# Kernel tuning notes

Measured on AMD Instinct MI355X. Metric: run time of the kernel, lower is better.

Reference implementation:

```python
import jax, jax.numpy as jnp
import numpy as np

RADIUS = 0.15
NSAMPLE = 128
NPOINT = 128
EPS = 1e-5  # BatchNorm eps (eval mode, running_mean=0, running_var=1)


def _bn(x, g, b):
    shape = (1, -1) + (1,) * (x.ndim - 2)
    return x * (g / jnp.sqrt(1.0 + EPS)).reshape(shape) + b.reshape(shape)


def _fps(x, npoint):
    # farthest point sampling; x: (Bk, N, 3) -> (Bk, npoint) int32
    Bn, N, _ = x.shape

    def step(carry, _):
        dist, far = carry
        c = jnp.take_along_axis(x, far[:, None, None], 1)  # (Bk,1,3)
        d = jnp.sum((x - c) ** 2, -1)
        dist = jnp.minimum(dist, d)
        return (dist, jnp.argmax(dist, -1).astype(jnp.int32)), far

    init = (jnp.full((Bn, N), 1e10, x.dtype), jnp.zeros((Bn,), jnp.int32))
    _, idxs = jax.lax.scan(step, init, None, length=npoint)
    return idxs.T  # (Bk, npoint)


def _sa_module(x, f, mlp):
    # PointnetSAModuleVotes: FPS -> ball query -> group (use_xyz, normalize_xyz)
    # -> shared MLP (conv2d 1x1 + BN + ReLU) -> max over nsample.
    Bk, M, _ = x.shape
    fps_idx = _fps(x, NPOINT)
    new_xyz = jnp.take_along_axis(x, fps_idx[..., None], 1)  # (Bk,np,3)
    d2 = jnp.sum((new_xyz[:, :, None, :] - x[:, None, :, :]) ** 2, -1)  # (Bk,np,M)
    cand = jnp.where(d2 < RADIUS ** 2, jnp.arange(M)[None, None, :], M)
    cand = jnp.sort(cand, -1)[..., :NSAMPLE]  # first nsample in-radius indices
    first = cand[..., :1]
    first = jnp.where(first == M, 0, first)
    idx = jnp.where(cand == M, first, cand)  # (Bk,np,ns), pad with first valid
    gx = jnp.take_along_axis(x, idx.reshape(Bk, -1)[..., None], 1).reshape(Bk, NPOINT, NSAMPLE, 3)
    gxn = (gx - new_xyz[:, :, None, :]) / RADIUS  # normalize_xyz=True
    gf = jnp.take_along_axis(f[:, :, None, :], idx[:, None, :, :], 3)  # (Bk,C,np,ns)
    h = jnp.concatenate([gxn.transpose(0, 3, 1, 2), gf], 1)  # (Bk, C+3, np, ns)
    for (w, b, g, be) in mlp:
        h = jax.nn.relu(_bn(jnp.einsum('oc,bcps->bops', w, h) + b[None, :, None, None], g, be))
    return new_xyz, h.max(-1)  # (Bk,np,3), (Bk,128,np)


def setup_inputs() -> dict:
    key = jax.random.key(0)
    ks = iter(jax.random.split(key, 40))
    B, M, K, C = 2, 1024, 19, 256
    inp = {}
    inp['xyz'] = jax.random.normal(next(ks), (B, M, K, 3), jnp.float32)
    inp['features'] = jax.random.normal(next(ks), (B, C, K, M), jnp.float32)

    def conv_p(prefix, cin, cout):
        inp[prefix + '_w'] = jax.random.normal(next(ks), (cout, cin), jnp.float32) * (1.0 / np.sqrt(cin))
        inp[prefix + '_b'] = jax.random.normal(next(ks), (cout,), jnp.float32) * 0.02
        inp[prefix + '_g'] = 1.0 + 0.1 * jax.random.normal(next(ks), (cout,), jnp.float32)
        inp[prefix + '_be'] = 0.02 * jax.random.normal(next(ks), (cout,), jnp.float32)

    conv_p('m1', C + 3, 128)  # use_xyz -> 259 in-channels
    conv_p('m2', 128, 128)
    conv_p('m3', 128, 128)
    conv_p('c1', 128, 128)
    conv_p('c2', 128, 128)
    inp['op_w'] = jax.random.normal(next(ks), (K, 5, 128), jnp.float32) * (1.0 / np.sqrt(128))
    inp['op_b'] = jax.random.normal(next(ks), (K, 5), jnp.float32) * 0.02
    return inp


def reference(xyz, features, m1_w, m1_b, m1_g, m1_be, m2_w, m2_b, m2_g, m2_be,
              m3_w, m3_b, m3_g, m3_be, c1_w, c1_b, c1_g, c1_be,
              c2_w, c2_b, c2_g, c2_be, op_w, op_b):
    B, M, K, _ = xyz.shape
    C = features.shape[1]
    # fold vote_factor k into the batch dim (all per-k SA/conv weights are shared)
    x = xyz.transpose(0, 2, 1, 3).reshape(B * K, M, 3)
    f = features.transpose(0, 2, 1, 3).reshape(B * K, C, M)
    mlp = [(m1_w, m1_b, m1_g, m1_be), (m2_w, m2_b, m2_g, m2_be), (m3_w, m3_b, m3_g, m3_be)]
    new_xyz, feat = _sa_module(x, f, mlp)
    net = jax.nn.relu(_bn(jnp.einsum('oc,bcp->bop', c1_w, feat) + c1_b[None, :, None], c1_g, c1_be))
    net = jax.nn.relu(_bn(jnp.einsum('oc,bcp->bop', c2_w, net) + c2_b[None, :, None], c2_g, c2_be))
    net = net.reshape(B, K, 128, NPOINT)
    # per-k output conv (conv_op ModuleList), 128 -> 2+3
    out = jnp.einsum('koc,bkcp->bkop', op_w, net) + op_b[None, :, :, None]
    net_t = out.transpose(0, 1, 3, 2)  # (B,K,np,5)
    agg_xyz = new_xyz.reshape(B, K, NPOINT, 3)
    center = agg_xyz + net_t[..., 2:5]  # decode_scores_
    scores = jnp.concatenate([net_t[..., :2], center], -1)  # obj(2) + center(3)
    return scores, agg_xyz, feat.reshape(B, K, 128, NPOINT)
```

## Files before the change

### kernel.cpp

```cpp
#include <hip/hip_runtime.h>
#include <math.h>

#define NBK   38

#define OFF_XC    0u
#define OFF_NXYZ  466944u
#define OFF_BIDX  525312u
#define OFF_W1F   3015680u
#define OFF_PREP  22938624u
#define OFF_WF    22955008u
#define OFF_CNT   23348224u

#define OUT_AGG   24320
#define OUT_FEAT  38912

typedef short bf16x8 __attribute__((ext_vector_type(8)));
typedef float f32x4  __attribute__((ext_vector_type(4)));
typedef int   v4i    __attribute__((ext_vector_type(4)));
typedef int   v2i    __attribute__((ext_vector_type(2)));

__device__ __forceinline__ float dist2f(float a0, float a1, float a2,
                                        float b0, float b1, float b2) {
#pragma clang fp contract(off)
  float d0 = a0 - b0;
  float d1 = a1 - b1;
  float d2 = a2 - b2;
  return d0 * d0 + d1 * d1 + d2 * d2;
}

__device__ __forceinline__ void split2rn(float v, unsigned& sh, unsigned& sm) {
  unsigned u = __float_as_uint(v);
  unsigned rh = (u + 0x7fffu + ((u >> 16) & 1u)) & 0xffff0000u;
  sh = rh >> 16;
  float r1 = v - __uint_as_float(rh);
  unsigned u1 = __float_as_uint(r1);
  unsigned rm = (u1 + 0x7fffu + ((u1 >> 16) & 1u)) & 0xffff0000u;
  sm = rm >> 16;
}

__global__ __launch_bounds__(1024, 4) void front_kernel(
    const float* __restrict__ xyz, const float* __restrict__ feats,
    const float* __restrict__ m1w, const float* __restrict__ m1b,
    const float* __restrict__ m1g, const float* __restrict__ m1be,
    const float* __restrict__ m2w, const float* __restrict__ m2b,
    const float* __restrict__ m2g, const float* __restrict__ m2be,
    const float* __restrict__ m3w, const float* __restrict__ m3b,
    const float* __restrict__ m3g, const float* __restrict__ m3be,
    const float* __restrict__ c1w, const float* __restrict__ c1b,
    const float* __restrict__ c1g, const float* __restrict__ c1be,
    const float* __restrict__ c2w, const float* __restrict__ c2b,
    const float* __restrict__ c2g, const float* __restrict__ c2be,
    float* __restrict__ xc, float* __restrict__ nxyz, float* __restrict__ agg,
    int* __restrict__ bidx, int* __restrict__ counts,
    float* __restrict__ W1f, short* __restrict__ Wf, float* __restrict__ prep)
{
  __shared__ __align__(16) char smem[32768];
  int bid = blockIdx.x, t = threadIdx.x;
  int wave = t >> 6, lane = t & 63;

  if (bid < NBK) {
    int bk = bid;
    int b = bk / 19, k = bk % 19;
    float* sx0 = (float*)smem;
    float* sx1 = sx0 + 1024;
    float* sx2 = sx1 + 1024;
    float* scen = sx2 + 1024;
    float* sd = scen + 384;
    int* si = (int*)(sd + 16);
    int* sfar = si + 16;

    const float* src = xyz + ((size_t)((b * 1024 + t) * 19 + k)) * 3;
    float x0 = src[0], x1 = src[1], x2 = src[2];
    sx0[t] = x0; sx1[t] = x1; sx2[t] = x2;
    xc[(bk * 3 + 0) * 1024 + t] = x0;
    xc[(bk * 3 + 1) * 1024 + t] = x1;
    xc[(bk * 3 + 2) * 1024 + t] = x2;
    if (t == 0) *sfar = 0;
    float dist = 1e10f;
    __syncthreads();

    for (int it = 0; it < 128; ++it) {
      int far = *sfar;
      float c0 = sx0[far], c1 = sx1[far], c2 = sx2[far];
      if (t < 3) scen[it * 3 + t] = (t == 0) ? c0 : ((t == 1) ? c1 : c2);
      float d = dist2f(x0, x1, x2, c0, c1, c2);
      dist = fminf(dist, d);
      float dmax = dist;
#pragma unroll
      for (int off = 1; off <= 32; off <<= 1)
        dmax = fmaxf(dmax, __shfl_xor(dmax, off));
      unsigned long long mk = __ballot(dist == dmax);
      if (lane == 0) {
        sd[wave] = dmax;
        si[wave] = (wave << 6) + __builtin_ctzll(mk);
      }
      __syncthreads();
      if (t < 16) {
        float dw = sd[t]; int iw = si[t];
        unsigned long long key =
            ((unsigned long long)__float_as_uint(dw) << 32) | (unsigned)(1023 - iw);
#pragma unroll
        for (int off = 8; off >= 1; off >>= 1) {
          unsigned hi = (unsigned)(key >> 32), lo = (unsigned)key;
          unsigned h2 = __shfl_xor(hi, off);
          unsigned l2 = __shfl_xor(lo, off);
          unsigned long long ok = ((unsigned long long)h2 << 32) | l2;
          if (ok > key) key = ok;
        }
        if (t == 0) *sfar = 1023 - (int)(key & 0xffffffffu);
      }
      __syncthreads();
    }

    if (t < 384) {
      float v = scen[t];
      nxyz[bk * 384 + t] = v;
      agg[bk * 384 + t]  = v;
    }

    for (int p = wave * 8; p < wave * 8 + 8; ++p) {
      float c0 = scen[p * 3 + 0], c1 = scen[p * 3 + 1], c2 = scen[p * 3 + 2];
      int* outp = bidx + ((size_t)(bk * 128 + p)) * 128;
      int count = 0, first = 0;
      bool got = false;
      for (int ch = 0; ch < 16 && count < 128; ++ch) {
        int m = (ch << 6) + lane;
        float d = dist2f(sx0[m], sx1[m], sx2[m], c0, c1, c2);
        bool flag = d < 0.0225f;
        unsigned long long mask = __ballot(flag);
        if (!got && mask) { first = (ch << 6) + __builtin_ctzll(mask); got = true; }
        int pos = count + (int)__popcll(mask & ((1ull << lane) - 1ull));
        if (flag && pos < 128) outp[pos] = m;
        count += (int)__popcll(mask);
      }
      for (int j = count + lane; j < 128; j += 64) outp[j] = first;
      if (lane == 0) counts[bk * 128 + p] = count > 128 ? 128 : count;
    }
    return;
  }

  if (bid < 342) {
    short* ffrag = (short*)smem;
    if (t >= 256) {
      for (int i = 0; i < 8; ++i) __syncthreads();
      return;
    }
    int blk = bid - NBK;
    int bk = blk >> 3, m0 = (blk & 7) << 7;
    int b = bk / 19, k = bk % 19;
    int quad = lane >> 4, nl = lane & 15;
    int mloc = t & 127, chalf = t >> 7;
    int st_w = mloc >> 4, sl_w = mloc & 15;
    const float* fbase = feats + ((size_t)(b * 4864 + k)) * 1024 + m0 + mloc;

    f32x4 acc[2][8];
#pragma unroll
    for (int oi = 0; oi < 2; ++oi)
#pragma unroll
      for (int st = 0; st < 8; ++st) acc[oi][st] = (f32x4){0.f, 0.f, 0.f, 0.f};

    for (int ch = 0; ch < 4; ++ch) {
      int cbase = ch * 64 + chalf * 32;
#pragma unroll
      for (int g = 0; g < 4; ++g) {
        float v[8];
#pragma unroll
        for (int j = 0; j < 8; ++j)
          v[j] = fbase[(size_t)(cbase + g * 8 + j) * 19456];
        unsigned sh[8], sm[8];
#pragma unroll
        for (int j = 0; j < 8; ++j) split2rn(v[j], sh[j], sm[j]);
        int base = chalf * 4096 + st_w * 512 + (g * 16 + sl_w) * 8;
        v4i ph = {(int)(sh[0] | (sh[1] << 16)), (int)(sh[2] | (sh[3] << 16)),
                  (int)(sh[4] | (sh[5] << 16)), (int)(sh[6] | (sh[7] << 16))};
        *(v4i*)&ffrag[base] = ph;
        v4i pm = {(int)(sm[0] | (sm[1] << 16)), (int)(sm[2] | (sm[3] << 16)),
                  (int)(sm[4] | (sm[5] << 16)), (int)(sm[6] | (sm[7] << 16))};
        *(v4i*)&ffrag[base + 8192] = pm;
      }
      __syncthreads();
#pragma unroll
      for (int kkl = 0; kkl < 2; ++kkl) {
        int kk = ch * 2 + kkl;
        bf16x8 a[2][2];
#pragma unroll
        for (int oi = 0; oi < 2; ++oi) {
          int o_row = (wave * 2 + oi) * 16 + nl;
          const float* wsrc = m1w + o_row * 259 + 3 + kk * 32 + quad * 8;
          float wv[8];
#pragma unroll
          for (int j = 0; j < 8; ++j) wv[j] = wsrc[j];
          unsigned sh[8], sm[8];
#pragma unroll
          for (int j = 0; j < 8; ++j) split2rn(wv[j], sh[j], sm[j]);
          short ah[8], am[8];
#pragma unroll
          for (int j = 0; j < 8; ++j) { ah[j] = (short)sh[j]; am[j] = (short)sm[j]; }
          a[oi][0] = (bf16x8){ah[0], ah[1], ah[2], ah[3], ah[4], ah[5], ah[6], ah[7]};
          a[oi][1] = (bf16x8){am[0], am[1], am[2], am[3], am[4], am[5], am[6], am[7]};
        }
#pragma unroll
        for (int st = 0; st < 8; ++st) {
          const short* hb = ffrag + kkl * 4096 + st * 512 + lane * 8;
          bf16x8 b0 = *(const bf16x8*)hb;
          bf16x8 b1 = *(const bf16x8*)(hb + 8192);
#pragma unroll
          for (int oi = 0; oi < 2; ++oi) {
            f32x4 c = acc[oi][st];
            c = __builtin_amdgcn_mfma_f32_16x16x32_bf16(a[oi][1], b0, c, 0, 0, 0);
            c = __builtin_amdgcn_mfma_f32_16x16x32_bf16(a[oi][0], b1, c, 0, 0, 0);
            c = __builtin_amdgcn_mfma_f32_16x16x32_bf16(a[oi][0], b0, c, 0, 0, 0);
            acc[oi][st] = c;
          }
        }
      }
      __syncthreads();
    }
    float inv = 1.0f / sqrtf(1.0f + 1e-5f);
#pragma unroll
    for (int oi = 0; oi < 2; ++oi) {
      int o0 = (wave * 2 + oi) * 16 + quad * 4;
      float4 bb = *(const float4*)&m1b[o0];
      float4 gg = *(const float4*)&m1g[o0];
#pragma unroll
      for (int st = 0; st < 8; ++st) {
        int m_out = m0 + st * 16 + nl;
        f32x4 cc = acc[oi][st];
        float4 r;
        r.x = (cc[0] + bb.x) * (gg.x * inv);
        r.y = (cc[1] + bb.y) * (gg.y * inv);
        r.z = (cc[2] + bb.z) * (gg.z * inv);
        r.w = (cc[3] + bb.w) * (gg.w * inv);
        *(float4*)&W1f[((size_t)(bk * 1024 + m_out)) * 128 + o0] = r;
      }
    }
    return;
  }

  if (bid < 350) {
    int idx = (bid - 342) * 1024 + t;
#pragma unroll
    for (int e = 0; e < 4; ++e) {
      int i = idx * 4 + e;
      int c = i & 127, o = (i >> 7) & 127, l = i >> 14;
      float w = (l ? m3w : m2w)[o * 128 + c];
      unsigned sh, sm;
      split2rn(w, sh, sm);
      int ot = o >> 4, mm = o & 15, kk = c >> 5, q = (c & 31) >> 3, j = c & 7;
      int within = (q * 16 + mm) * 8 + j;
      Wf[(((l * 2 + 0) * 4 + kk) * 8 + ot) * 512 + within] = (short)sh;
      Wf[(((l * 2 + 1) * 4 + kk) * 8 + ot) * 512 + within] = (short)sm;
    }
    return;
  }

  if (bid < 358) {
    int idx2 = (bid - 350) * 1024 + t;
#pragma unroll
    for (int e = 0; e < 4; ++e) {
      int i = idx2 * 4 + e;
      int c = i & 127, o = (i >> 7) & 127, l = i >> 14;
      float w = (l ? c2w : c1w)[o * 128 + c];
      unsigned sh, sm;
      split2rn(w, sh, sm);
      int ot = o >> 4, mm = o & 15, kk = c >> 5, q = (c & 31) >> 3, j = c & 7;
      int within = (q * 16 + mm) * 8 + j;
      Wf[131072 + (((l * 2 + 0) * 4 + kk) * 8 + ot) * 512 + within] = (short)sh;
      Wf[131072 + (((l * 2 + 1) * 4 + kk) * 8 + ot) * 512 + within] = (short)sm;
    }
    return;
  }

  if (t < 128) {
    float inv = 1.0f / sqrtf(1.0f + 1e-5f);
    float a1 = m1g[t] * inv;
    prep[t] = a1;
    float a2 = m2g[t] * inv;  prep[256 + t] = a2;  prep[384 + t] = fmaf(m2b[t], a2, m2be[t]);
    float a3 = m3g[t] * inv;  prep[512 + t] = a3;  prep[640 + t] = fmaf(m3b[t], a3, m3be[t]);
    float ac1 = c1g[t] * inv; prep[768 + t] = ac1; prep[896 + t] = fmaf(c1b[t], ac1, c1be[t]);
    float ac2 = c2g[t] * inv; prep[1024 + t] = ac2; prep[1152 + t] = fmaf(c2b[t], ac2, c2be[t]);
    prep[1280 + 4 * t + 0] = m1w[t * 259 + 0] * a1;
    prep[1280 + 4 * t + 1] = m1w[t * 259 + 1] * a1;
    prep[1280 + 4 * t + 2] = m1w[t * 259 + 2] * a1;
    prep[1280 + 4 * t + 3] = m1be[t];
  }
}

__device__ __forceinline__ void mfma_layer(const short* __restrict__ Wf,
                                           const short* hfrag, int l,
                                           int wave, int lane, int nst_h,
                                           f32x4 acc[2][4])
{
#pragma unroll 1
  for (int kk = 0; kk < 4; ++kk) {
    bf16x8 a[2][2];
#pragma unroll
    for (int oi = 0; oi < 2; ++oi)
#pragma unroll
      for (int sp = 0; sp < 2; ++sp)
        a[oi][sp] = *(const bf16x8*)(Wf + (((l * 2 + sp) * 4 + kk) * 8 + (wave * 2 + oi)) * 512 + lane * 8);
    for (int st = 0; st < nst_h; ++st) {
      const short* hb = hfrag + kk * 2048 + st * 512 + lane * 8;
      bf16x8 b0 = *(const bf16x8*)(hb);
      bf16x8 b1 = *(const bf16x8*)(hb + 8192);
#pragma unroll
      for (int oi = 0; oi < 2; ++oi) {
        f32x4 c = acc[oi][st];
        c = __builtin_amdgcn_mfma_f32_16x16x32_bf16(a[oi][1], b0, c, 0, 0, 0);
        c = __builtin_amdgcn_mfma_f32_16x16x32_bf16(a[oi][0], b1, c, 0, 0, 0);
        c = __builtin_amdgcn_mfma_f32_16x16x32_bf16(a[oi][0], b0, c, 0, 0, 0);
        acc[oi][st] = c;
      }
    }
  }
}

__global__ __launch_bounds__(256, 3) void sa_kernel(
    const float* __restrict__ xc, const float* __restrict__ nxyz,
    const int* __restrict__ bidx, const int* __restrict__ counts,
    const float* __restrict__ W1f, const float* __restrict__ prep,
    const short* __restrict__ Wf, float* __restrict__ feat_out)
{
  __shared__ __align__(16) short hfrag[16384];
  __shared__ float pcs[512];
  __shared__ float sm[32 * 128];
  __shared__ float ccen[12];
  __shared__ int scnt[4];
  int gb = blockIdx.x, bk = gb >> 5, pb = (gb & 31) << 2;
  int t = threadIdx.x;
  int wave = t >> 6, lane = t & 63;
  int quad = lane >> 4, nl = lane & 15;

  pcs[t] = prep[1280 + t];
  pcs[256 + t] = prep[1536 + t];
  if (t < 4) scnt[t] = counts[bk * 128 + pb + t];
  if (t < 12) {
    int bb = t / 3, c = t % 3;
    ccen[t] = nxyz[(bk * 128 + pb + bb) * 3 + c];
  }
  __syncthreads();
  int n0 = (scnt[0] + 15) >> 4, n1 = (scnt[1] + 15) >> 4;
  int n2 = (scnt[2] + 15) >> 4, n3 = (scnt[3] + 15) >> 4;
  int pf1 = n0, pf2 = n0 + n1, pf3 = n0 + n1 + n2, T = n0 + n1 + n2 + n3;

  for (int q0 = 0; q0 < T; q0 += 4) {
    int nst_h = T - q0;
    if (nst_h > 4) nst_h = 4;
    {
      int cg = wave;
      int st = lane >> 4, sl = lane & 15;
      if (st < nst_h) {
        int q = q0 + st;
        int bq = (q >= pf1) + (q >= pf2) + (q >= pf3);
        int tstart = (bq == 0) ? 0 : (bq == 1) ? pf1 : (bq == 2) ? pf2 : pf3;
        int tslot = q - tstart;
        int m = bidx[((size_t)(bk * 128 + pb + bq)) * 128 + tslot * 16 + sl];
        float cen0 = ccen[bq * 3 + 0], cen1 = ccen[bq * 3 + 1], cen2 = ccen[bq * 3 + 2];
        float g0 = (xc[(bk * 3 + 0) * 1024 + m] - cen0) * (1.0f / 0.15f);
        float g1 = (xc[(bk * 3 + 1) * 1024 + m] - cen1) * (1.0f / 0.15f);
        float g2 = (xc[(bk * 3 + 2) * 1024 + m] - cen2) * (1.0f / 0.15f);
        const float4* wrow = (const float4*)(W1f + ((size_t)(bk * 1024 + m)) * 128 + cg * 32);
        const float4* pcp = (const float4*)pcs + cg * 32;
#pragma unroll
        for (int g = 0; g < 4; ++g) {
          float4 wva = wrow[g * 2], wvb = wrow[g * 2 + 1];
          float wv[8] = {wva.x, wva.y, wva.z, wva.w, wvb.x, wvb.y, wvb.z, wvb.w};
          unsigned sh[8], smv[8];
#pragma unroll
          for (int e = 0; e < 8; ++e) {
            float4 pc = pcp[g * 8 + e];
            float hv = fmaxf(wv[e] + pc.x * g0 + pc.y * g1 + pc.z * g2 + pc.w, 0.f);
            split2rn(hv, sh[e], smv[e]);
          }
          int base = (cg * 4 + st) * 512 + (g * 16 + sl) * 8;
          v4i ph = {(int)(sh[0] | (sh[1] << 16)), (int)(sh[2] | (sh[3] << 16)),
                    (int)(sh[4] | (sh[5] << 16)), (int)(sh[6] | (sh[7] << 16))};
          *(v4i*)&hfrag[base] = ph;
          v4i pm = {(int)(smv[0] | (smv[1] << 16)), (int)(smv[2] | (smv[3] << 16)),
                    (int)(smv[4] | (smv[5] << 16)), (int)(smv[6] | (smv[7] << 16))};
          *(v4i*)&hfrag[base + 8192] = pm;
        }
      }
    }
    __syncthreads();

    f32x4 acc[2][4];
#pragma unroll
    for (int oi = 0; oi < 2; ++oi)
#pragma unroll
      for (int st = 0; st < 4; ++st) acc[oi][st] = (f32x4){0.f, 0.f, 0.f, 0.f};
    mfma_layer(Wf, hfrag, 0, wave, lane, nst_h, acc);
    __syncthreads();

#pragma unroll
    for (int oi = 0; oi < 2; ++oi) {
      int o0 = (wave * 2 + oi) * 16 + quad * 4;
      float4 al = *(const float4*)&prep[256 + o0];
      float4 be = *(const float4*)&prep[384 + o0];
      int kk2 = o0 >> 5, g2 = (o0 & 31) >> 3, j0 = o0 & 7;
      for (int st = 0; st < nst_h; ++st) {
        f32x4 cc = acc[oi][st];
        float v0 = fmaxf(fmaf(cc[0], al.x, be.x), 0.f);
        float v1 = fmaxf(fmaf(cc[1], al.y, be.y), 0.f);
        float v2 = fmaxf(fmaf(cc[2], al.z, be.z), 0.f);
        float v3 = fmaxf(fmaf(cc[3], al.w, be.w), 0.f);
        unsigned h0, m0_, h1, m1_, h2, m2_, h3, m3_;
        split2rn(v0, h0, m0_); split2rn(v1, h1, m1_);
        split2rn(v2, h2, m2_); split2rn(v3, h3, m3_);
        int base = (kk2 * 4 + st) * 512 + (g2 * 16 + nl) * 8 + j0;
        v2i w0 = {(int)(h0 | (h1 << 16)), (int)(h2 | (h3 << 16))};
        *(v2i*)&hfrag[base] = w0;
        v2i w1 = {(int)(m0_ | (m1_ << 16)), (int)(m2_ | (m3_ << 16))};
        *(v2i*)&hfrag[base + 8192] = w1;
      }
    }
    __syncthreads();

#pragma unroll
    for (int oi = 0; oi < 2; ++oi)
#pragma unroll
      for (int st = 0; st < 4; ++st) acc[oi][st] = (f32x4){0.f, 0.f, 0.f, 0.f};
    mfma_layer(Wf, hfrag, 1, wave, lane, nst_h, acc);

#pragma unroll
    for (int oi = 0; oi < 2; ++oi) {
      int o0 = (wave * 2 + oi) * 16 + quad * 4;
      float4 al = *(const float4*)&prep[512 + o0];
      float4 be = *(const float4*)&prep[640 + o0];
      for (int st = 0; st < nst_h; ++st) {
        f32x4 cc = acc[oi][st];
        float v[4];
        v[0] = fmaxf(fmaf(cc[0], al.x, be.x), 0.f);
        v[1] = fmaxf(fmaf(cc[1], al.y, be.y), 0.f);
        v[2] = fmaxf(fmaf(cc[2], al.z, be.z), 0.f);
        v[3] = fmaxf(fmaf(cc[3], al.w, be.w), 0.f);
#pragma unroll
        for (int r = 0; r < 4; ++r) {
          float x = v[r];
          x = fmaxf(x, __shfl_xor(x, 1));
          x = fmaxf(x, __shfl_xor(x, 2));
          x = fmaxf(x, __shfl_xor(x, 4));
          x = fmaxf(x, __shfl_xor(x, 8));
          if (nl == 0) sm[(q0 + st) * 128 + o0 + r] = x;
        }
      }
    }
    __syncthreads();
  }

#pragma unroll
  for (int e = t; e < 512; e += 256) {
    int bb = e >> 7, o = e & 127;
    int qs = (bb == 0) ? 0 : (bb == 1) ? pf1 : (bb == 2) ? pf2 : pf3;
    int nq = (bb == 0) ? n0 : (bb == 1) ? n1 : (bb == 2) ? n2 : n3;
    float v = sm[qs * 128 + o];
    for (int q = 1; q < nq; ++q) v = fmaxf(v, sm[(qs + q) * 128 + o]);
    feat_out[(((size_t)bk) << 14) + (o << 7) + pb + bb] = v;
  }
}

__global__ __launch_bounds__(256) void head_kernel(const float* __restrict__ featg,
    const float* __restrict__ prep, const short* __restrict__ Wf,
    const float* __restrict__ nxyz, const float* __restrict__ opw,
    const float* __restrict__ opb, float* __restrict__ scores)
{
  __shared__ __align__(16) short hfrag[16384];
  __shared__ float hplain[128 * 65];
  int bk = blockIdx.x >> 1, p0 = (blockIdx.x & 1) << 6;
  int t = threadIdx.x;
  int wave = t >> 6, lane = t & 63;
  int quad = lane >> 4, nl = lane & 15;
  const short* WC = Wf + 131072;

  {
    int cg = wave;
    int st = lane >> 4, sl = lane & 15;
    const float* fb = featg + (bk << 14) + p0 + lane;
#pragma unroll
    for (int g = 0; g < 4; ++g) {
      float v[8];
#pragma unroll
      for (int e = 0; e < 8; ++e)
        v[e] = fb[(cg * 32 + g * 8 + e) << 7];
      unsigned sh[8], sm[8];
#pragma unroll
      for (int e = 0; e < 8; ++e) split2rn(v[e], sh[e], sm[e]);
      int base = (cg * 4 + st) * 512 + (g * 16 + sl) * 8;
      v4i ph = {(int)(sh[0] | (sh[1] << 16)), (int)(sh[2] | (sh[3] << 16)),
                (int)(sh[4] | (sh[5] << 16)), (int)(sh[6] | (sh[7] << 16))};
      *(v4i*)&hfrag[base] = ph;
      v4i pm = {(int)(sm[0] | (sm[1] << 16)), (int)(sm[2] | (sm[3] << 16)),
                (int)(sm[4] | (sm[5] << 16)), (int)(sm[6] | (sm[7] << 16))};
      *(v4i*)&hfrag[base + 8192] = pm;
    }
  }
  __syncthreads();

  f32x4 acc[2][4];
#pragma unroll
  for (int oi = 0; oi < 2; ++oi)
#pragma unroll
    for (int st = 0; st < 4; ++st) acc[oi][st] = (f32x4){0.f, 0.f, 0.f, 0.f};
  mfma_layer(WC, hfrag, 0, wave, lane, 4, acc);
  __syncthreads();

#pragma unroll
  for (int oi = 0; oi < 2; ++oi) {
    int o0 = (wave * 2 + oi) * 16 + quad * 4;
    float4 al = *(const float4*)&prep[768 + o0];
    float4 be = *(const float4*)&prep[896 + o0];
    int kk2 = o0 >> 5, g2 = (o0 & 31) >> 3, j0 = o0 & 7;
#pragma unroll
    for (int st = 0; st < 4; ++st) {
      f32x4 cc = acc[oi][st];
      float v0 = fmaxf(fmaf(cc[0], al.x, be.x), 0.f);
      float v1 = fmaxf(fmaf(cc[1], al.y, be.y), 0.f);
      float v2 = fmaxf(fmaf(cc[2], al.z, be.z), 0.f);
      float v3 = fmaxf(fmaf(cc[3], al.w, be.w), 0.f);
      unsigned h0, m0_, h1, m1_, h2, m2_, h3, m3_;
      split2rn(v0, h0, m0_); split2rn(v1, h1, m1_);
      split2rn(v2, h2, m2_); split2rn(v3, h3, m3_);
      int base = (kk2 * 4 + st) * 512 + (g2 * 16 + nl) * 8 + j0;
      v2i w0 = {(int)(h0 | (h1 << 16)), (int)(h2 | (h3 << 16))};
      *(v2i*)&hfrag[base] = w0;
      v2i w1 = {(int)(m0_ | (m1_ << 16)), (int)(m2_ | (m3_ << 16))};
      *(v2i*)&hfrag[base + 8192] = w1;
    }
  }
  __syncthreads();

#pragma unroll
  for (int oi = 0; oi < 2; ++oi)
#pragma unroll
    for (int st = 0; st < 4; ++st) acc[oi][st] = (f32x4){0.f, 0.f, 0.f, 0.f};
  mfma_layer(WC, hfrag, 1, wave, lane, 4, acc);

#pragma unroll
  for (int oi = 0; oi < 2; ++oi) {
    int o0 = (wave * 2 + oi) * 16 + quad * 4;
    float4 al = *(const float4*)&prep[1024 + o0];
    float4 be = *(const float4*)&prep[1152 + o0];
#pragma unroll
    for (int st = 0; st < 4; ++st) {
      f32x4 cc = acc[oi][st];
      int p = st * 16 + nl;
      hplain[(o0 + 0) * 65 + p] = fmaxf(fmaf(cc[0], al.x, be.x), 0.f);
      hplain[(o0 + 1) * 65 + p] = fmaxf(fmaf(cc[1], al.y, be.y), 0.f);
      hplain[(o0 + 2) * 65 + p] = fmaxf(fmaf(cc[2], al.z, be.z), 0.f);
      hplain[(o0 + 3) * 65 + p] = fmaxf(fmaf(cc[3], al.w, be.w), 0.f);
    }
  }
  __syncthreads();

  if (t < 64) {
    int p = t, k = bk % 19;
    float res[5];
#pragma unroll
    for (int j = 0; j < 5; ++j) {
      const float* wr = opw + ((size_t)(k * 5 + j)) * 128;
      float a = opb[k * 5 + j];
      for (int c = 0; c < 128; ++c) a = fmaf(wr[c], hplain[c * 65 + p], a);
      res[j] = a;
    }
    int pg = p0 + p;
    float a0 = nxyz[(bk * 128 + pg) * 3 + 0];
    float a1 = nxyz[(bk * 128 + pg) * 3 + 1];
    float a2 = nxyz[(bk * 128 + pg) * 3 + 2];
    float* sc = scores + ((size_t)(bk * 128 + pg)) * 5;
    sc[0] = res[0];
    sc[1] = res[1];
    sc[2] = a0 + res[2];
    sc[3] = a1 + res[3];
    sc[4] = a2 + res[4];
  }
}

extern "C" void kernel_launch(void* const* d_in, const int* in_sizes, int n_in,
                              void* d_out, int out_size, void* d_ws, size_t ws_size,
                              hipStream_t stream) {
  (void)in_sizes; (void)n_in; (void)out_size; (void)ws_size;
  const float* xyz  = (const float*)d_in[0];
  const float* fts  = (const float*)d_in[1];
  const float* m1w  = (const float*)d_in[2];
  const float* m1b  = (const float*)d_in[3];
  const float* m1g  = (const float*)d_in[4];
  const float* m1be = (const float*)d_in[5];
  const float* m2w  = (const float*)d_in[6];
  const float* m2b  = (const float*)d_in[7];
  const float* m2g  = (const float*)d_in[8];
  const float* m2be = (const float*)d_in[9];
  const float* m3w  = (const float*)d_in[10];
  const float* m3b  = (const float*)d_in[11];
  const float* m3g  = (const float*)d_in[12];
  const float* m3be = (const float*)d_in[13];
  const float* c1w  = (const float*)d_in[14];
  const float* c1b  = (const float*)d_in[15];
  const float* c1g  = (const float*)d_in[16];
  const float* c1be = (const float*)d_in[17];
  const float* c2w  = (const float*)d_in[18];
  const float* c2b  = (const float*)d_in[19];
  const float* c2g  = (const float*)d_in[20];
  const float* c2be = (const float*)d_in[21];
  const float* opw  = (const float*)d_in[22];
  const float* opb  = (const float*)d_in[23];

  float* out = (float*)d_out;
  char* ws = (char*)d_ws;
  float* xc   = (float*)(ws + OFF_XC);
  float* nxyz = (float*)(ws + OFF_NXYZ);
  int*   bidx = (int*)(ws + OFF_BIDX);
  float* W1f  = (float*)(ws + OFF_W1F);
  float* prep = (float*)(ws + OFF_PREP);
  short* Wf   = (short*)(ws + OFF_WF);
  int*   cnt  = (int*)(ws + OFF_CNT);

  hipLaunchKernelGGL(front_kernel, dim3(359), dim3(1024), 0, stream,
                     xyz, fts, m1w, m1b, m1g, m1be, m2w, m2b, m2g, m2be,
                     m3w, m3b, m3g, m3be, c1w, c1b, c1g, c1be,
                     c2w, c2b, c2g, c2be,
                     xc, nxyz, out + OUT_AGG, bidx, cnt, W1f, Wf, prep);
  hipLaunchKernelGGL(sa_kernel, dim3(NBK * 32), dim3(256), 0, stream,
                     xc, nxyz, bidx, cnt, W1f, prep, Wf, out + OUT_FEAT);
  hipLaunchKernelGGL(head_kernel, dim3(NBK * 2), dim3(256), 0, stream,
                     out + OUT_FEAT, prep, Wf, nxyz, opw, opb, out);
}
```

Before: 298.9 us.

## Run farthest point sampling in a single wave with per-lane point registers

Result: no change. 295.4 us (-1.1%).

```diff
diff --git a/kernel.cpp b/kernel.cpp
--- a/kernel.cpp
+++ b/kernel.cpp
@@ -64,53 +64,72 @@
     float* sx0 = (float*)smem;
     float* sx1 = sx0 + 1024;
     float* sx2 = sx1 + 1024;
-    float* scen = sx2 + 1024;
-    float* sd = scen + 384;
-    int* si = (int*)(sd + 16);
-    int* sfar = si + 16;
+    float* sp0 = sx2 + 1024;
+    float* sp1 = sp0 + 1088;
+    float* sp2 = sp1 + 1088;
+    float* scen = sp2 + 1088;
 
     const float* src = xyz + ((size_t)((b * 1024 + t) * 19 + k)) * 3;
     float x0 = src[0], x1 = src[1], x2 = src[2];
     sx0[t] = x0; sx1[t] = x1; sx2[t] = x2;
+    int tp = t + (t >> 4);
+    sp0[tp] = x0; sp1[tp] = x1; sp2[tp] = x2;
     xc[(bk * 3 + 0) * 1024 + t] = x0;
     xc[(bk * 3 + 1) * 1024 + t] = x1;
     xc[(bk * 3 + 2) * 1024 + t] = x2;
-    if (t == 0) *sfar = 0;
-    float dist = 1e10f;
     __syncthreads();
 
-    for (int it = 0; it < 128; ++it) {
-      int far = *sfar;
-      float c0 = sx0[far], c1 = sx1[far], c2 = sx2[far];
-      if (t < 3) scen[it * 3 + t] = (t == 0) ? c0 : ((t == 1) ? c1 : c2);
-      float d = dist2f(x0, x1, x2, c0, c1, c2);
-      dist = fminf(dist, d);
-      float dmax = dist;
-#pragma unroll
-      for (int off = 1; off <= 32; off <<= 1)
-        dmax = fmaxf(dmax, __shfl_xor(dmax, off));
-      unsigned long long mk = __ballot(dist == dmax);
-      if (lane == 0) {
-        sd[wave] = dmax;
-        si[wave] = (wave << 6) + __builtin_ctzll(mk);
-      }
-      __syncthreads();
-      if (t < 16) {
-        float dw = sd[t]; int iw = si[t];
-        unsigned long long key =
-            ((unsigned long long)__float_as_uint(dw) << 32) | (unsigned)(1023 - iw);
-#pragma unroll
-        for (int off = 8; off >= 1; off >>= 1) {
-          unsigned hi = (unsigned)(key >> 32), lo = (unsigned)key;
-          unsigned h2 = __shfl_xor(hi, off);
-          unsigned l2 = __shfl_xor(lo, off);
-          unsigned long long ok = ((unsigned long long)h2 << 32) | l2;
-          if (ok > key) key = ok;
-        }
-        if (t == 0) *sfar = 1023 - (int)(key & 0xffffffffu);
-      }
-      __syncthreads();
-    }
+    if (wave == 0) {
+      float px[16], py[16], pz[16], dist[16];
+      int base = lane * 17;
+#pragma unroll
+      for (int j = 0; j < 16; ++j) {
+        px[j] = sp0[base + j];
+        py[j] = sp1[base + j];
+        pz[j] = sp2[base + j];
+        dist[j] = 1e10f;
+      }
+      int far = 0;
+      for (int it = 0; it < 128; ++it) {
+        int fa = far + (far >> 4);
+        float c0 = sp0[fa], c1 = sp1[fa], c2 = sp2[fa];
+        if (lane == 0) {
+          scen[it * 3 + 0] = c0;
+          scen[it * 3 + 1] = c1;
+          scen[it * 3 + 2] = c2;
+        }
+#pragma unroll
+        for (int j = 0; j < 16; ++j) {
+          float d = dist2f(px[j], py[j], pz[j], c0, c1, c2);
+          dist[j] = fminf(dist[j], d);
+        }
+        float tv[8]; int tj[8];
+#pragma unroll
+        for (int i = 0; i < 8; ++i) {
+          bool L = dist[2 * i] >= dist[2 * i + 1];
+          tv[i] = L ? dist[2 * i] : dist[2 * i + 1];
+          tj[i] = L ? (2 * i) : (2 * i + 1);
+        }
+#pragma unroll
+        for (int s = 1; s < 8; s <<= 1) {
+#pragma unroll
+          for (int i = 0; i < 8; i += 2 * s) {
+            bool L = tv[i] >= tv[i + s];
+            tv[i] = L ? tv[i] : tv[i + s];
+            tj[i] = L ? tj[i] : tj[i + s];
+          }
+        }
+        float lmax = tv[0];
+        float g = lmax;
+#pragma unroll
+        for (int off = 1; off <= 32; off <<= 1)
+          g = fmaxf(g, __shfl_xor(g, off));
+        unsigned long long mk = __ballot(lmax == g);
+        int wl = __builtin_ctzll(mk);
+        far = __shfl((lane << 4) + tj[0], wl);
+      }
+    }
+    __syncthreads();
 
     if (t < 384) {
       float v = scen[t];
```
